# Optimization experiments

Hardware: AMD Instinct MI355X
Metric: run time of the kernel (lower is better)

## Reference

```python
import jax, jax.numpy as jnp
import numpy as np

DT = 0.01
NT = 2000
B = 16384


def setup_inputs() -> dict:
    key = jax.random.key(0)
    k1, k2 = jax.random.split(key)
    x0 = jax.random.normal(k1, (B, 3), dtype=jnp.float32)
    p = jax.random.uniform(k2, (3,), dtype=jnp.float32) * 10.0  # matches torch.rand(3)*10
    return {"x0": x0, "p": p}


def _yp(X, p):
    # Lorenz RHS, X: [B, 3]
    x, y, z = X[:, 0], X[:, 1], X[:, 2]
    return jnp.stack([p[0] * (y - x), x * (p[1] - z) - y, x * y - p[2] * z], axis=1)


def reference(x0, p):
    dt = jnp.float32(DT)

    def step(Xi, _):
        k1 = _yp(Xi, p)
        k2 = _yp(Xi + dt / 2 * k1, p)
        k3 = _yp(Xi + dt / 2 * k2, p)
        k4 = _yp(Xi + dt * k3, p)
        Xn = Xi + dt / 6 * (k1 + 2 * k2 + 2 * k3 + k4)
        return Xn, Xn

    _, traj = jax.lax.scan(step, x0, None, length=NT)  # [NT, B, 3]
    X = jnp.concatenate([x0[None], traj], axis=0)      # [NT+1, B, 3]
    return jnp.transpose(X, (1, 2, 0))                  # [B, 3, NT+1]
```

## Files before the change

### kernel.cpp

```cpp
#include <hip/hip_runtime.h>


#define NT     2000
#define TT     32
#define NFULL  62
#define TAIL   16
#define TROWS  2001
#define ROWS   64
#define LROWS  65

#define FMA(a,b,c) __builtin_fmaf((a),(b),(c))

__global__ __launch_bounds__(128) void lorenz_rk4(
    const float* __restrict__ x0,
    const float* __restrict__ p,
    float* __restrict__ out)
{
#pragma clang fp contract(off)
    __shared__ float buf[2][3][TT][LROWS];

    const int tid  = threadIdx.x;
    const int lane = tid & 63;
    const int b0   = blockIdx.x * ROWS;

    if (tid < 64) {
        const float p0  = p[0], p1 = p[1], p2n = -p[2];
        const float h1 = 0.01f;
        const float h2 = 0.01f / 2.0f;
        const float h6 = 0.01f / 6.0f;
        const int b = b0 + lane;
        float x = x0[3*b + 0], y = x0[3*b + 1], z = x0[3*b + 2];

        {
            size_t g = (size_t)b * (3 * TROWS);
            out[g] = x; out[g + TROWS] = y; out[g + 2*TROWS] = z;
        }

#define STEP() do {                                                          \
        float k1x = p0 * (y - x);                                            \
        float k1y = FMA(x, p1 - z, -y);                                      \
        float k1z = FMA(p2n, z, x * y);                                      \
        float ax = FMA(h2,k1x,x), ay = FMA(h2,k1y,y), az = FMA(h2,k1z,z);    \
        float k2x = p0 * (ay - ax);                                          \
        float k2y = FMA(ax, p1 - az, -ay);                                   \
        float k2z = FMA(p2n, az, ax * ay);                                   \
        float bx = FMA(h2,k2x,x), by = FMA(h2,k2y,y), bz = FMA(h2,k2z,z);    \
        float k3x = p0 * (by - bx);                                          \
        float k3y = FMA(bx, p1 - bz, -by);                                   \
        float k3z = FMA(p2n, bz, bx * by);                                   \
        float cx = FMA(h1,k3x,x), cy = FMA(h1,k3y,y), cz = FMA(h1,k3z,z);    \
        float k4x = p0 * (cy - cx);                                          \
        float k4y = FMA(cx, p1 - cz, -cy);                                   \
        float k4z = FMA(p2n, cz, cx * cy);                                   \
        float sx = FMA(2.0f,k2x,k1x); sx = FMA(2.0f,k3x,sx); sx += k4x;      \
        float sy = FMA(2.0f,k2y,k1y); sy = FMA(2.0f,k3y,sy); sy += k4y;      \
        float sz = FMA(2.0f,k2z,k1z); sz = FMA(2.0f,k3z,sz); sz += k4z;      \
        x = FMA(h6,sx,x); y = FMA(h6,sy,y); z = FMA(h6,sz,z);                \
    } while (0)

        for (int k = 0; k < NFULL; ++k) {
            float* bb = &buf[k & 1][0][0][0];
#pragma unroll
            for (int tl = 0; tl < TT; ++tl) {
                STEP();
                bb[              tl*LROWS + lane] = x;
                bb[  TT*LROWS  + tl*LROWS + lane] = y;
                bb[2*TT*LROWS  + tl*LROWS + lane] = z;
            }
            __syncthreads();
        }
#pragma unroll
        for (int tl = 0; tl < TAIL; ++tl) {
            STEP();
            buf[0][0][tl][lane] = x;
            buf[0][1][tl][lane] = y;
            buf[0][2][tl][lane] = z;
        }
        __syncthreads();
#undef STEP
    } else {
        for (int k = 0; k < NFULL; ++k) {
            __syncthreads();
            const float* bb = &buf[k & 1][0][0][0];
            const int tloc = lane & 31;
            int rloc = lane >> 5;
            size_t g = (size_t)(b0 + rloc) * (3 * TROWS) + 1 + k * TT + tloc;
#pragma unroll 8
            for (int rp = 0; rp < 32; ++rp) {
                float vx = bb[              tloc*LROWS + rloc];
                float vy = bb[  TT*LROWS  + tloc*LROWS + rloc];
                float vz = bb[2*TT*LROWS  + tloc*LROWS + rloc];
                out[g]             = vx;
                out[g +     TROWS] = vy;
                out[g + 2 * TROWS] = vz;
                rloc += 2;
                g    += (size_t)2 * (3 * TROWS);
            }
        }
        __syncthreads();
        {
            const int tloc = lane & 15;
            int rloc = lane >> 4;
            size_t g = (size_t)(b0 + rloc) * (3 * TROWS) + 1 + NFULL * TT + tloc;
#pragma unroll 8
            for (int rp = 0; rp < 16; ++rp) {
                float vx = buf[0][0][tloc][rloc];
                float vy = buf[0][1][tloc][rloc];
                float vz = buf[0][2][tloc][rloc];
                out[g]             = vx;
                out[g +     TROWS] = vy;
                out[g + 2 * TROWS] = vz;
                rloc += 4;
                g    += (size_t)4 * (3 * TROWS);
            }
        }
    }
}

extern "C" void kernel_launch(void* const* d_in, const int* in_sizes, int n_in,
                              void* d_out, int out_size, void* d_ws, size_t ws_size,
                              hipStream_t stream)
{
    const float* x0  = (const float*)d_in[0];
    const float* p   = (const float*)d_in[1];
    float*       out = (float*)d_out;

    const int B = in_sizes[0] / 3;
    const int nblocks = B / ROWS;

    lorenz_rk4<<<nblocks, 128, 0, stream>>>(x0, p, out);
}
```

Measured before the change: 171.2 us.

## Use two store wavefronts and 64-step tiles for trajectory writeback

Doubles the time tile to 64 steps, halving the number of block barriers, and adds a second store wavefront (192 threads) so each store wave handles 32 rows. Each store lane now writes one time step across its rows, giving 64-wide contiguous writes per row. Shared memory doubles to about 100KB per block, which can cut the number of resident blocks per CU. The compute loop is only partly unrolled (16), which may add loop overhead on the serial integration path.

Measured after the change: 172.9 us. About the same (+1.1%).

```diff
diff --git a/kernel.cpp b/kernel.cpp
--- a/kernel.cpp
+++ b/kernel.cpp
@@ -2,8 +2,8 @@
 
 
 #define NT     2000
-#define TT     32
-#define NFULL  62
+#define TT     64
+#define NFULL  31
 #define TAIL   16
 #define TROWS  2001
 #define ROWS   64
@@ -11,7 +11,7 @@
 
 #define FMA(a,b,c) __builtin_fmaf((a),(b),(c))
 
-__global__ __launch_bounds__(128) void lorenz_rk4(
+__global__ __launch_bounds__(192) void lorenz_rk4(
     const float* __restrict__ x0,
     const float* __restrict__ p,
     float* __restrict__ out)
@@ -60,7 +60,7 @@
 
         for (int k = 0; k < NFULL; ++k) {
             float* bb = &buf[k & 1][0][0][0];
-#pragma unroll
+#pragma unroll 16
             for (int tl = 0; tl < TT; ++tl) {
                 STEP();
                 bb[              tl*LROWS + lane] = x;
@@ -69,47 +69,42 @@
             }
             __syncthreads();
         }
-#pragma unroll
+#pragma unroll 16
         for (int tl = 0; tl < TAIL; ++tl) {
             STEP();
-            buf[0][0][tl][lane] = x;
-            buf[0][1][tl][lane] = y;
-            buf[0][2][tl][lane] = z;
+            buf[1][0][tl][lane] = x;
+            buf[1][1][tl][lane] = y;
+            buf[1][2][tl][lane] = z;
         }
         __syncthreads();
 #undef STEP
     } else {
+        const int w     = (tid >> 6) - 1;
+        const int rbase = w * 32;
+        const int t     = lane;
+
         for (int k = 0; k < NFULL; ++k) {
             __syncthreads();
             const float* bb = &buf[k & 1][0][0][0];
-            const int tloc = lane & 31;
-            int rloc = lane >> 5;
-            size_t g = (size_t)(b0 + rloc) * (3 * TROWS) + 1 + k * TT + tloc;
-#pragma unroll 8
-            for (int rp = 0; rp < 32; ++rp) {
-                float vx = bb[              tloc*LROWS + rloc];
-                float vy = bb[  TT*LROWS  + tloc*LROWS + rloc];
-                float vz = bb[2*TT*LROWS  + tloc*LROWS + rloc];
-                out[g]             = vx;
-                out[g +     TROWS] = vy;
-                out[g + 2 * TROWS] = vz;
-                rloc += 2;
-                g    += (size_t)2 * (3 * TROWS);
+            size_t g = (size_t)(b0 + rbase) * (3 * TROWS) + 1 + (size_t)k * TT + t;
+#pragma unroll 4
+            for (int r = rbase; r < rbase + 32; ++r) {
+                out[g]             = bb[              t*LROWS + r];
+                out[g +     TROWS] = bb[  TT*LROWS  + t*LROWS + r];
+                out[g + 2 * TROWS] = bb[2*TT*LROWS  + t*LROWS + r];
+                g += (size_t)(3 * TROWS);
             }
         }
         __syncthreads();
         {
             const int tloc = lane & 15;
-            int rloc = lane >> 4;
-            size_t g = (size_t)(b0 + rloc) * (3 * TROWS) + 1 + NFULL * TT + tloc;
-#pragma unroll 8
-            for (int rp = 0; rp < 16; ++rp) {
-                float vx = buf[0][0][tloc][rloc];
-                float vy = buf[0][1][tloc][rloc];
-                float vz = buf[0][2][tloc][rloc];
-                out[g]             = vx;
-                out[g +     TROWS] = vy;
-                out[g + 2 * TROWS] = vz;
+            int rloc = rbase + (lane >> 4);
+            size_t g = (size_t)(b0 + rloc) * (3 * TROWS) + 1 + (size_t)NFULL * TT + tloc;
+#pragma unroll 4
+            for (int i = 0; i < 8; ++i) {
+                out[g]             = buf[1][0][tloc][rloc];
+                out[g +     TROWS] = buf[1][1][tloc][rloc];
+                out[g + 2 * TROWS] = buf[1][2][tloc][rloc];
                 rloc += 4;
                 g    += (size_t)4 * (3 * TROWS);
             }
@@ -128,5 +123,5 @@
     const int B = in_sizes[0] / 3;
     const int nblocks = B / ROWS;
 
-    lorenz_rk4<<<nblocks, 128, 0, stream>>>(x0, p, out);
+    lorenz_rk4<<<nblocks, 192, 0, stream>>>(x0, p, out);
 }
```
